# Performance work log

Hardware: AMD Instinct MI355X
Metric: run time of the kernel (lower is better)

The kernel has to match this reference:

```python
import jax, jax.numpy as jnp
import numpy as np

B, T, C, H = 2, 2048, 1024, 16
HS = C // H  # head_size = 64
EPS = 1e-5


def _ln(x, g, b):
    m = jnp.mean(x, axis=-1, keepdims=True)
    v = jnp.mean(jnp.square(x - m), axis=-1, keepdims=True)
    return (x - m) * jax.lax.rsqrt(v + EPS) * g + b


def setup_inputs() -> dict:
    key = jax.random.key(0)
    ks = jax.random.split(key, 16)
    s = lambda k, shape, fan: jax.random.normal(k, shape, jnp.float32) * (fan ** -0.5)
    return {
        "x": jax.random.normal(ks[0], (B, T, C), jnp.float32),
        "Wq": s(ks[1], (H, C, HS), C), "bq": jnp.zeros((H, HS), jnp.float32),
        "Wk": s(ks[2], (H, C, HS), C), "bk": jnp.zeros((H, HS), jnp.float32),
        "Wv": s(ks[3], (H, C, HS), C), "bv": jnp.zeros((H, HS), jnp.float32),
        "Wo": s(ks[4], (C, C), C), "bo": jnp.zeros((C,), jnp.float32),
        "g1": jnp.ones((C,), jnp.float32), "b1": jnp.zeros((C,), jnp.float32),
        "g2": jnp.ones((C,), jnp.float32), "b2": jnp.zeros((C,), jnp.float32),
        "W1": s(ks[5], (C, C), C), "bf1": jnp.zeros((C,), jnp.float32),
        "W2": s(ks[6], (C, C), C), "bf2": jnp.zeros((C,), jnp.float32),
    }


def _block(x, Wq, bq, Wk, bk, Wv, bv, Wo, bo, g1, b1, g2, b2, W1, bf1, W2, bf2):
    h = _ln(x, g1, b1)
    # per-head projections, batched over heads: (B,T,C) x (H,C,HS) -> (B,H,T,HS)
    q = jnp.einsum('btc,hcd->bhtd', h, Wq) + bq[None, :, None, :]
    k = jnp.einsum('btc,hcd->bhtd', h, Wk) + bk[None, :, None, :]
    v = jnp.einsum('btc,hcd->bhtd', h, Wv) + bv[None, :, None, :]
    w = jnp.einsum('bhqd,bhkd->bhqk', q, k) * (HS ** -0.5)
    causal = jnp.tril(jnp.ones((T, T), bool))  # tril[q,k]==0 -> -inf
    w = jnp.where(causal[None, None], w, -jnp.inf)
    # FAITHFUL quirk: original uses F.softmax(w, dim=1) on (B,T,T),
    # i.e. normalization over the QUERY axis (axis=2 of bhqk).
    w = jax.nn.softmax(w, axis=2)
    att = jnp.einsum('bhqk,bhkd->bhqd', w, v)
    att = att.transpose(0, 2, 1, 3).reshape(x.shape[0], x.shape[1], -1)  # concat heads
    x = x + att @ Wo + bo
    h2 = _ln(x, g2, b2)
    x = x + jax.nn.relu(h2 @ W1 + bf1) @ W2 + bf2
    return x


def reference(x, Wq, bq, Wk, bk, Wv, bv, Wo, bo, g1, b1, g2, b2, W1, bf1, W2, bf2):
    return _block(x, Wq, bq, Wk, bk, Wv, bv, Wo, bo, g1, b1, g2, b2, W1, bf1, W2, bf2)
```

## Files before the change

kernel.cpp:

```cpp
#include <hip/hip_runtime.h>
#include <hip/hip_bf16.h>
#include <math.h>


#define B_   2
#define T_   2048
#define C_   1024
#define H_   16
#define HS_  64
#define NROWS 4096
#define C3   3072
#define K1C  0.1803368801111244f

typedef unsigned short ushort_t;
typedef __attribute__((ext_vector_type(8))) short short8;
typedef __attribute__((ext_vector_type(4))) float f32x4;
typedef __attribute__((ext_vector_type(16))) float f32x16;

__device__ __forceinline__ ushort_t f2bf(float f) {
  __hip_bfloat16 h = __float2bfloat16(f);
  ushort_t u; __builtin_memcpy(&u, &h, 2); return u;
}
__device__ __forceinline__ float bf2f(ushort_t u) {
  union { unsigned u; float f; } v; v.u = ((unsigned)u) << 16;
  return v.f;
}
__device__ __forceinline__ unsigned pk2(float a, float b) {
  __hip_bfloat162 t = __float22bfloat162_rn(make_float2(a, b));
  unsigned u; __builtin_memcpy(&u, &t, 4); return u;
}
__device__ __forceinline__ unsigned pkhw(float a, float b) {
  unsigned u;
  asm("v_cvt_pk_bf16_f32 %0, %1, %2" : "=v"(u) : "v"(a), "v"(b));
  return u;
}
__device__ __forceinline__ short8 mk8(unsigned a, unsigned b, unsigned c, unsigned d) {
  union { unsigned u[4]; short8 s; } t;
  t.u[0] = a; t.u[1] = b; t.u[2] = c; t.u[3] = d; return t.s;
}
__device__ __forceinline__ void pl32swap(unsigned &a, unsigned &b) {
  asm("v_permlane32_swap_b32 %0, %1" : "+v"(a), "+v"(b));
}
__device__ __forceinline__ f32x4 mfma16(short8 a, short8 b, f32x4 c) {
  return __builtin_amdgcn_mfma_f32_16x16x32_bf16(a, b, c, 0, 0, 0);
}
__device__ __forceinline__ f32x16 mfma32(short8 a, short8 b, f32x16 c) {
  return __builtin_amdgcn_mfma_f32_32x32x16_bf16(a, b, c, 0, 0, 0);
}
typedef const __attribute__((address_space(1))) void g_void;
typedef __attribute__((address_space(3))) void l_void;
__device__ __forceinline__ void gl_lds16(const void* g, void* l) {
  __builtin_amdgcn_global_load_lds((g_void*)g, (l_void*)l, 16, 0, 0);
}

__global__ __launch_bounds__(256) void ln_bf16(
    const float* __restrict__ x, const float* __restrict__ g,
    const float* __restrict__ b, ushort_t* __restrict__ out) {
  int row = blockIdx.x;
  const float* xr = x + (size_t)row * C_;
  int t = threadIdx.x;
  float4 v = ((const float4*)xr)[t];
  float s  = v.x + v.y + v.z + v.w;
  float ss = v.x*v.x + v.y*v.y + v.z*v.z + v.w*v.w;
  #pragma unroll
  for (int off = 32; off > 0; off >>= 1) {
    s  += __shfl_down(s, off);
    ss += __shfl_down(ss, off);
  }
  __shared__ float red[2][4];
  int wid = t >> 6, lane = t & 63;
  if (lane == 0) { red[0][wid] = s; red[1][wid] = ss; }
  __syncthreads();
  if (t == 0) {
    float a = 0, c = 0;
    for (int i = 0; i < 4; i++) { a += red[0][i]; c += red[1][i]; }
    red[0][0] = a; red[1][0] = c;
  }
  __syncthreads();
  float mean = red[0][0] * (1.0f / C_);
  float var  = red[1][0] * (1.0f / C_) - mean * mean;
  float r = rsqrtf(var + 1e-5f);
  float4 gv = ((const float4*)g)[t];
  float4 bv = ((const float4*)b)[t];
  ushort4 o;
  o.x = f2bf((v.x - mean) * r * gv.x + bv.x);
  o.y = f2bf((v.y - mean) * r * gv.y + bv.y);
  o.z = f2bf((v.z - mean) * r * gv.z + bv.z);
  o.w = f2bf((v.w - mean) * r * gv.w + bv.w);
  ((ushort4*)(out + (size_t)row * C_))[t] = o;
}

__global__ __launch_bounds__(256) void prep_weights(
    const float* __restrict__ Wq, const float* __restrict__ Wk,
    const float* __restrict__ Wv, const float* __restrict__ Wo,
    const float* __restrict__ W1, const float* __restrict__ W2,
    const float* __restrict__ bq, const float* __restrict__ bk,
    const float* __restrict__ bv, ushort_t* __restrict__ Wqkvt,
    ushort_t* __restrict__ Wot3, float* __restrict__ bqkv) {
  int bid = blockIdx.x;
  if (bid < 12288) {
    int idx = bid * 256 + threadIdx.x;
    int n = idx >> 10, c = idx & 1023;
    int sel = n >> 10, nn = n & 1023;
    const float* W = (sel == 0) ? Wq : ((sel == 1) ? Wk : Wv);
    Wqkvt[idx] = f2bf(W[((size_t)(nn >> 6) * C_ + c) * HS_ + (nn & 63)]);
  } else if (bid < 24576) {
    int idx = (bid - 12288) * 256 + threadIdx.x;
    int sel = idx >> 20, rem = idx & 1048575;
    int n = rem >> 10, k = rem & 1023;
    const float* W = (sel == 0) ? Wo : ((sel == 1) ? W1 : W2);
    Wot3[idx] = f2bf(W[(size_t)k * C_ + n]);
  } else {
    int i = (bid - 24576) * 256 + threadIdx.x;
    if (i < 3072)
      bqkv[i] = (i < 1024) ? bq[i] : ((i < 2048) ? bk[i - 1024] : bv[i - 2048]);
  }
}

__global__ __launch_bounds__(256) void gemm128q(
    const ushort_t* __restrict__ A, const ushort_t* __restrict__ Bt,
    const float* __restrict__ bias, ushort_t* __restrict__ Cm,
    int M, int N, int K) {
  __shared__ ushort_t As[128 * 32];
  __shared__ ushort_t Bs[128 * 32];
  int t = threadIdx.x;
  int m0 = blockIdx.y * 128, n0 = blockIdx.x * 128;
  int w = t >> 6, l = t & 63;
  int wr = w >> 1, wc = w & 1;
  int lo = l & 15, hi = l >> 4;
  f32x4 acc[4][4] = {};
  int srow = t >> 2, scol = (t & 3) * 8;
  const ushort_t* Ag = A  + (size_t)(m0 + srow) * K + scol;
  const ushort_t* Bg = Bt + (size_t)(n0 + srow) * K + scol;
  ushort_t* AsP = As + t * 8;
  ushort_t* BsP = Bs + t * 8;
  for (int k0 = 0; k0 < K; k0 += 32) {
    gl_lds16(Ag + k0,          AsP);
    gl_lds16(Ag + 64 * K + k0, AsP + 64 * 32);
    gl_lds16(Bg + k0,          BsP);
    gl_lds16(Bg + 64 * K + k0, BsP + 64 * 32);
    __syncthreads();
    short8 af[4], bfr[4];
    #pragma unroll
    for (int i = 0; i < 4; i++)
      af[i] = *(const short8*)&As[(wr * 64 + i * 16 + lo) * 32 + hi * 8];
    #pragma unroll
    for (int j = 0; j < 4; j++)
      bfr[j] = *(const short8*)&Bs[(wc * 64 + j * 16 + lo) * 32 + hi * 8];
    #pragma unroll
    for (int i = 0; i < 4; i++)
      #pragma unroll
      for (int j = 0; j < 4; j++)
        acc[i][j] = mfma16(af[i], bfr[j], acc[i][j]);
    __syncthreads();
  }
  float qs = (n0 < C_) ? K1C : 1.0f;
  #pragma unroll
  for (int i = 0; i < 4; i++) {
    int m = m0 + wr * 64 + i * 16 + hi * 4;
    #pragma unroll
    for (int j = 0; j < 4; j++) {
      int n = n0 + wc * 64 + j * 16 + lo;
      float bv = bias[n];
      #pragma unroll
      for (int r = 0; r < 4; r++)
        Cm[(size_t)(m + r) * N + n] = f2bf((acc[i][j][r] + bv) * qs);
    }
  }
}

template<int OUT_BF16, int RELU, int HAS_RES>
__global__ __launch_bounds__(256) void gemm64(
    const ushort_t* __restrict__ A, const ushort_t* __restrict__ Bt,
    const float* __restrict__ bias, const float* __restrict__ res,
    void* __restrict__ Cm, int M, int N, int K) {
  __shared__ ushort_t As[128 * 32];
  __shared__ ushort_t Bs[64 * 32];
  int t = threadIdx.x;
  int m0 = blockIdx.y * 128, n0 = blockIdx.x * 64;
  int w = t >> 6, l = t & 63;
  int wr = w >> 1, wc = w & 1;
  int lo = l & 15, hi = l >> 4;
  f32x4 acc[4][2] = {};
  int srow = t >> 2, scol = (t & 3) * 8;
  const ushort_t* Ag = A  + (size_t)(m0 + srow) * K + scol;
  const ushort_t* Bg = Bt + (size_t)(n0 + srow) * K + scol;
  ushort_t* AsP = As + t * 8;
  ushort_t* BsP = Bs + t * 8;
  for (int k0 = 0; k0 < K; k0 += 32) {
    gl_lds16(Ag + k0,          AsP);
    gl_lds16(Ag + 64 * K + k0, AsP + 64 * 32);
    gl_lds16(Bg + k0,          BsP);
    __syncthreads();
    short8 af[4], bfr[2];
    #pragma unroll
    for (int i = 0; i < 4; i++)
      af[i] = *(const short8*)&As[(wr * 64 + i * 16 + lo) * 32 + hi * 8];
    #pragma unroll
    for (int j = 0; j < 2; j++)
      bfr[j] = *(const short8*)&Bs[(wc * 32 + j * 16 + lo) * 32 + hi * 8];
    #pragma unroll
    for (int i = 0; i < 4; i++)
      #pragma unroll
      for (int j = 0; j < 2; j++)
        acc[i][j] = mfma16(af[i], bfr[j], acc[i][j]);
    __syncthreads();
  }
  #pragma unroll
  for (int i = 0; i < 4; i++) {
    int m = m0 + wr * 64 + i * 16 + hi * 4;
    #pragma unroll
    for (int j = 0; j < 2; j++) {
      int n = n0 + wc * 32 + j * 16 + lo;
      float bv = bias[n];
      #pragma unroll
      for (int r = 0; r < 4; r++) {
        float v = acc[i][j][r] + bv;
        if (HAS_RES) v += res[(size_t)(m + r) * N + n];
        if (RELU) v = fmaxf(v, 0.f);
        if (OUT_BF16) ((ushort_t*)Cm)[(size_t)(m + r) * N + n] = f2bf(v);
        else          ((float*)Cm)[(size_t)(m + r) * N + n] = v;
      }
    }
  }
}

__global__ __launch_bounds__(256) void attn_stats(
    const ushort_t* __restrict__ QKV, float* __restrict__ dinv) {
  int bid = blockIdx.x;
  int xcd = bid & 7, loc = (bid >> 3) & 31, half = bid >> 8;
  int bh = xcd * 4 + (loc & 3);
  int j = loc >> 2;
  int kb = half ? (15 - j) : j;
  int b = bh >> 4, h = bh & 15;
  int t = threadIdx.x, w = t >> 6, l = t & 63, l31 = l & 31, hi32 = l >> 5;
  __shared__ ushort_t Qs[2][32 * 64];
  const ushort_t* Qb = QKV + (size_t)b * T_ * C3 + h * HS_;
  const ushort_t* Kb = Qb + C_;
  int k0w = kb * 128 + w * 32;
  short8 ka[4];
  #pragma unroll
  for (int c = 0; c < 4; c++)
    ka[c] = *(const short8*)(Kb + (size_t)(k0w + l31) * C3 + c * 16 + hi32 * 8);
  float s[16];
  #pragma unroll
  for (int r = 0; r < 16; r++) s[r] = 0.f;

  int qoff[4];
  #pragma unroll
  for (int c = 0; c < 4; c++)
    qoff[c] = l31 * 64 + ((c * 2 + hi32) ^ (l31 & 7)) * 8;
  const ushort_t* Q0 = &Qs[0][0];

  int sr = t >> 3, slot = t & 7, su = slot ^ (sr & 7);
  const ushort_t* Qsrc = Qb + (size_t)sr * C3 + su * 8;
  int qt0 = kb * 4, cnt = 64 - qt0;
  int dqt = qt0 + w;

  gl_lds16(Qsrc + (size_t)qt0 * 32 * C3, &Qs[0][t * 8]);
  for (int i = 0; i < cnt; i++) {
    int qt = qt0 + i, cur = i & 1;
    if (i + 1 < cnt) {
      gl_lds16(Qsrc + (size_t)(qt + 1) * 32 * C3, &Qs[cur ^ 1][t * 8]);
      asm volatile("s_waitcnt vmcnt(1)");
    } else {
      asm volatile("s_waitcnt vmcnt(0)");
    }
    __builtin_amdgcn_s_barrier();
    __builtin_amdgcn_sched_barrier(0);
    if (qt >= dqt) {
      int cb = cur << 11;
      short8 qf[4];
      #pragma unroll
      for (int c = 0; c < 4; c++)
        qf[c] = *(const short8*)(Q0 + cb + qoff[c]);
      __builtin_amdgcn_s_setprio(1);
      f32x16 d = {};
      #pragma unroll
      for (int c = 0; c < 4; c++) d = mfma32(ka[c], qf[c], d);
      __builtin_amdgcn_s_setprio(0);
      if (qt == dqt) {
        int qq = qt * 32 + l31;
        #pragma unroll
        for (int r = 0; r < 16; r++) {
          int k = k0w + (r & 3) + 8 * (r >> 2) + 4 * hi32;
          s[r] += (qq >= k) ? __builtin_amdgcn_exp2f(d[r]) : 0.f;
        }
      } else {
        #pragma unroll
        for (int r = 0; r < 16; r++) s[r] += __builtin_amdgcn_exp2f(d[r]);
      }
    }
    __builtin_amdgcn_sched_barrier(0);
    __builtin_amdgcn_s_barrier();
    __builtin_amdgcn_sched_barrier(0);
  }
  #pragma unroll
  for (int off = 1; off < 32; off <<= 1)
    #pragma unroll
    for (int r = 0; r < 16; r++)
      s[r] += __shfl_xor(s[r], off);
  if (l31 == 0) {
    #pragma unroll
    for (int r = 0; r < 16; r++) {
      int k = k0w + (r & 3) + 8 * (r >> 2) + 4 * hi32;
      dinv[(size_t)bh * T_ + k] = 1.0f / s[r];
    }
  }
}

__global__ __launch_bounds__(256) void transpose_v(
    const ushort_t* __restrict__ QKV, const float* __restrict__ dinv,
    ushort_t* __restrict__ Vt) {
  int t0 = blockIdx.x * 64;
  int bh = blockIdx.y; int b = bh >> 4, h = bh & 15;
  __shared__ ushort_t tile[64][65];
  int tid = threadIdx.x;
  #pragma unroll
  for (int i = 0; i < 16; i++) {
    int idx = i * 256 + tid;
    int tt = idx >> 6, dd = idx & 63;
    float v = bf2f(QKV[(size_t)(b * T_ + t0 + tt) * C3 + 2 * C_ + h * HS_ + dd]);
    tile[tt][dd] = f2bf(v * dinv[(size_t)bh * T_ + t0 + tt]);
  }
  __syncthreads();
  #pragma unroll
  for (int i = 0; i < 16; i++) {
    int idx = i * 256 + tid;
    int dd = idx >> 6, tt = idx & 63;
    Vt[((size_t)(bh * HS_ + dd)) * T_ + t0 + tt] = tile[tt][dd];
  }
}

__global__ __launch_bounds__(256) void attn_pv(
    const ushort_t* __restrict__ QKV, const ushort_t* __restrict__ Vt,
    ushort_t* __restrict__ att) {
  int bid = blockIdx.x;
  int xcd = bid & 7, loc = (bid >> 3) & 31, half = bid >> 8;
  int bh = xcd * 4 + (loc & 3);
  int j = loc >> 2;
  int qb = half ? j : (15 - j);
  int b = bh >> 4, h = bh & 15;
  int t = threadIdx.x, w = t >> 6, l = t & 63, l31 = l & 31, hi32 = l >> 5;
  __shared__ ushort_t KV[2][2][32 * 64];
  const ushort_t* Qb = QKV + (size_t)b * T_ * C3 + h * HS_;
  const ushort_t* Kb = Qb + C_;
  const ushort_t* Vb = Vt + (size_t)bh * HS_ * T_;
  int q0w = qb * 128 + w * 32;
  short8 qf[4];
  #pragma unroll
  for (int c = 0; c < 4; c++)
    qf[c] = *(const short8*)(Qb + (size_t)(q0w + l31) * C3 + c * 16 + hi32 * 8);
  f32x16 o0 = {}, o1 = {};
  int nkt = qb * 4 + 4;
  int dkt = q0w >> 5;

  int koff[4], voff[4];
  #pragma unroll
  for (int c = 0; c < 4; c++)
    koff[c] = l31 * 64 + ((c * 2 + hi32) ^ (l31 & 7)) * 8;
  #pragma unroll
  for (int i = 0; i < 4; i++) {
    int u = (i & 1) * 4 + (i >> 1) * 2 + hi32;
    voff[i] = 2048 + l31 * 64 + (u ^ (l31 & 7)) * 8;
  }
  const ushort_t* KV0 = &KV[0][0][0];

  int sr = t >> 3, slot = t & 7, su = slot ^ (sr & 7);
  int vdh = su >> 2, vc2 = su & 3;
  const ushort_t* Ksrc = Kb + (size_t)sr * C3 + su * 8;
  const ushort_t* Vsrc = Vb + (size_t)(vdh * 32 + sr) * T_ + vc2 * 8;

  gl_lds16(Ksrc, &KV[0][0][t * 8]);
  gl_lds16(Vsrc, &KV[0][1][t * 8]);
  for (int kt = 0; kt < nkt; kt++) {
    int cur = kt & 1;
    if (kt + 1 < nkt) {
      gl_lds16(Ksrc + (size_t)(kt + 1) * 32 * C3, &KV[cur ^ 1][0][t * 8]);
      gl_lds16(Vsrc + (kt + 1) * 32,              &KV[cur ^ 1][1][t * 8]);
      asm volatile("s_waitcnt vmcnt(2)");
    } else {
      asm volatile("s_waitcnt vmcnt(0)");
    }
    __builtin_amdgcn_s_barrier();
    __builtin_amdgcn_sched_barrier(0);
    if (kt <= dkt) {
      int cb = cur << 12;
      short8 ka[4], vf[4];
      #pragma unroll
      for (int c = 0; c < 4; c++)
        ka[c] = *(const short8*)(KV0 + cb + koff[c]);
      #pragma unroll
      for (int i = 0; i < 4; i++)
        vf[i] = *(const short8*)(KV0 + cb + voff[i]);
      __builtin_amdgcn_s_setprio(1);
      f32x16 sacc = {};
      #pragma unroll
      for (int c = 0; c < 4; c++) sacc = mfma32(ka[c], qf[c], sacc);
      __builtin_amdgcn_s_setprio(0);
      float e[16];
      if (kt == dkt) {
        int qq = q0w + l31;
        #pragma unroll
        for (int r = 0; r < 16; r++) {
          int k = kt * 32 + (r & 3) + 8 * (r >> 2) + 4 * hi32;
          e[r] = (k <= qq) ? __builtin_amdgcn_exp2f(sacc[r]) : 0.f;
        }
      } else {
        #pragma unroll
        for (int r = 0; r < 16; r++) e[r] = __builtin_amdgcn_exp2f(sacc[r]);
      }
      unsigned u[8];
      #pragma unroll
      for (int j2 = 0; j2 < 8; j2++) u[j2] = pkhw(e[2 * j2], e[2 * j2 + 1]);
      pl32swap(u[0], u[2]); pl32swap(u[1], u[3]);
      pl32swap(u[4], u[6]); pl32swap(u[5], u[7]);
      short8 pa0 = mk8(u[0], u[1], u[2], u[3]);
      short8 pa1 = mk8(u[4], u[5], u[6], u[7]);
      __builtin_amdgcn_s_setprio(1);
      o0 = mfma32(pa0, vf[0], o0);
      o1 = mfma32(pa0, vf[1], o1);
      o0 = mfma32(pa1, vf[2], o0);
      o1 = mfma32(pa1, vf[3], o1);
      __builtin_amdgcn_s_setprio(0);
    }
    __builtin_amdgcn_sched_barrier(0);
    __builtin_amdgcn_s_barrier();
    __builtin_amdgcn_sched_barrier(0);
  }

  #pragma unroll
  for (int r = 0; r < 16; r++) {
    int qq = q0w + (r & 3) + 8 * (r >> 2) + 4 * hi32;
    size_t base = (size_t)(b * T_ + qq) * C_ + h * HS_;
    att[base + l31]      = f2bf(o0[r]);
    att[base + 32 + l31] = f2bf(o1[r]);
  }
}

extern "C" void kernel_launch(void* const* d_in, const int* in_sizes, int n_in,
                              void* d_out, int out_size, void* d_ws, size_t ws_size,
                              hipStream_t stream) {
  const float* x   = (const float*)d_in[0];
  const float* Wq  = (const float*)d_in[1];
  const float* bq  = (const float*)d_in[2];
  const float* Wk  = (const float*)d_in[3];
  const float* bk  = (const float*)d_in[4];
  const float* Wv  = (const float*)d_in[5];
  const float* bv  = (const float*)d_in[6];
  const float* Wo  = (const float*)d_in[7];
  const float* bo  = (const float*)d_in[8];
  const float* g1  = (const float*)d_in[9];
  const float* b1  = (const float*)d_in[10];
  const float* g2  = (const float*)d_in[11];
  const float* b2  = (const float*)d_in[12];
  const float* W1  = (const float*)d_in[13];
  const float* bf1 = (const float*)d_in[14];
  const float* W2  = (const float*)d_in[15];
  const float* bf2 = (const float*)d_in[16];
  float* out = (float*)d_out;

  char* base = (char*)d_ws;
  const size_t MB = 1 << 20;
  ushort_t* QKVb  = (ushort_t*)(base);
  ushort_t* hb    = (ushort_t*)(base + 24 * MB);
  ushort_t* Vt    = (ushort_t*)(base + 32 * MB);
  float*    y     = (float*)   (base + 40 * MB);
  ushort_t* Wqkvt = (ushort_t*)(base + 56 * MB);
  ushort_t* Wot   = (ushort_t*)(base + 62 * MB);
  ushort_t* W1t   = (ushort_t*)(base + 64 * MB);
  ushort_t* W2t   = (ushort_t*)(base + 66 * MB);
  float*    bqkv  = (float*)   (base + 68 * MB);
  float*    dinv  = (float*)   (base + 68 * MB + 65536);

  prep_weights<<<24588, 256, 0, stream>>>(Wq, Wk, Wv, Wo, W1, W2,
                                          bq, bk, bv, Wqkvt, Wot, bqkv);

  ln_bf16<<<NROWS, 256, 0, stream>>>(x, g1, b1, hb);

  gemm128q<<<dim3(C3 / 128, NROWS / 128), 256, 0, stream>>>(
      hb, Wqkvt, bqkv, QKVb, NROWS, C3, C_);

  attn_stats<<<512, 256, 0, stream>>>(QKVb, dinv);
  transpose_v<<<dim3(T_ / 64, 32), 256, 0, stream>>>(QKVb, dinv, Vt);
  ushort_t* attb = hb;
  attn_pv<<<512, 256, 0, stream>>>(QKVb, Vt, attb);

  dim3 g64(C_ / 64, NROWS / 128);
  gemm64<0,0,1><<<g64, 256, 0, stream>>>(attb, Wot, bo, x, y, NROWS, C_, C_);

  ushort_t* h2b = QKVb;
  ln_bf16<<<NROWS, 256, 0, stream>>>(y, g2, b2, h2b);
  ushort_t* f1b = Vt;
  gemm64<1,1,0><<<g64, 256, 0, stream>>>(h2b, W1t, bf1, nullptr, f1b, NROWS, C_, C_);
  gemm64<0,0,1><<<g64, 256, 0, stream>>>(f1b, W2t, bf2, y, out, NROWS, C_, C_);
}
```

Before: 219.8 us.

## Process two tiles per barrier in attention kernels and swizzle QKV GEMM blocks per XCD

Both attention kernels now load two 32-row Q or K/V tiles per pipeline stage and process them in an unrolled pair. This halves the number of block-wide barriers and waitcnt stalls per tile, at the cost of doubled LDS usage. The QKV GEMM also moves from a 2D grid to a 1D grid with a mapping that gives each XCD a contiguous 8x12 block region, aiming for better L2 reuse. The unused pk2 helper is removed.

```diff
diff --git a/kernel.cpp b/kernel.cpp
--- a/kernel.cpp
+++ b/kernel.cpp
@@ -24,10 +24,6 @@
 __device__ __forceinline__ float bf2f(ushort_t u) {
   union { unsigned u; float f; } v; v.u = ((unsigned)u) << 16;
   return v.f;
-}
-__device__ __forceinline__ unsigned pk2(float a, float b) {
-  __hip_bfloat162 t = __float22bfloat162_rn(make_float2(a, b));
-  unsigned u; __builtin_memcpy(&u, &t, 4); return u;
 }
 __device__ __forceinline__ unsigned pkhw(float a, float b) {
   unsigned u;
@@ -124,7 +120,11 @@
   __shared__ ushort_t As[128 * 32];
   __shared__ ushort_t Bs[128 * 32];
   int t = threadIdx.x;
-  int m0 = blockIdx.y * 128, n0 = blockIdx.x * 128;
+  int bid = blockIdx.x;
+  int xcd = bid & 7, loc = bid >> 3;
+  int mb = (xcd >> 1) * 8 + (loc & 7);
+  int nb = (xcd & 1) * 12 + (loc >> 3);
+  int m0 = mb * 128, n0 = nb * 128;
   int w = t >> 6, l = t & 63;
   int wr = w >> 1, wc = w & 1;
   int lo = l & 15, hi = l >> 4;
@@ -234,7 +234,7 @@
   int kb = half ? (15 - j) : j;
   int b = bh >> 4, h = bh & 15;
   int t = threadIdx.x, w = t >> 6, l = t & 63, l31 = l & 31, hi32 = l >> 5;
-  __shared__ ushort_t Qs[2][32 * 64];
+  __shared__ ushort_t Qs[2][2][2048];
   const ushort_t* Qb = QKV + (size_t)b * T_ * C3 + h * HS_;
   const ushort_t* Kb = Qb + C_;
   int k0w = kb * 128 + w * 32;
@@ -250,45 +250,50 @@
   #pragma unroll
   for (int c = 0; c < 4; c++)
     qoff[c] = l31 * 64 + ((c * 2 + hi32) ^ (l31 & 7)) * 8;
-  const ushort_t* Q0 = &Qs[0][0];
 
   int sr = t >> 3, slot = t & 7, su = slot ^ (sr & 7);
   const ushort_t* Qsrc = Qb + (size_t)sr * C3 + su * 8;
   int qt0 = kb * 4, cnt = 64 - qt0;
   int dqt = qt0 + w;
 
-  gl_lds16(Qsrc + (size_t)qt0 * 32 * C3, &Qs[0][t * 8]);
-  for (int i = 0; i < cnt; i++) {
-    int qt = qt0 + i, cur = i & 1;
-    if (i + 1 < cnt) {
-      gl_lds16(Qsrc + (size_t)(qt + 1) * 32 * C3, &Qs[cur ^ 1][t * 8]);
-      asm volatile("s_waitcnt vmcnt(1)");
+  gl_lds16(Qsrc + (size_t)qt0 * 32 * C3,       &Qs[0][0][t * 8]);
+  gl_lds16(Qsrc + (size_t)(qt0 + 1) * 32 * C3, &Qs[0][1][t * 8]);
+  for (int i = 0; i < cnt; i += 2) {
+    int buf = (i >> 1) & 1;
+    if (i + 2 < cnt) {
+      gl_lds16(Qsrc + (size_t)(qt0 + i + 2) * 32 * C3, &Qs[buf ^ 1][0][t * 8]);
+      gl_lds16(Qsrc + (size_t)(qt0 + i + 3) * 32 * C3, &Qs[buf ^ 1][1][t * 8]);
+      asm volatile("s_waitcnt vmcnt(2)");
     } else {
       asm volatile("s_waitcnt vmcnt(0)");
     }
     __builtin_amdgcn_s_barrier();
     __builtin_amdgcn_sched_barrier(0);
-    if (qt >= dqt) {
-      int cb = cur << 11;
-      short8 qf[4];
-      #pragma unroll
-      for (int c = 0; c < 4; c++)
-        qf[c] = *(const short8*)(Q0 + cb + qoff[c]);
-      __builtin_amdgcn_s_setprio(1);
-      f32x16 d = {};
-      #pragma unroll
-      for (int c = 0; c < 4; c++) d = mfma32(ka[c], qf[c], d);
-      __builtin_amdgcn_s_setprio(0);
-      if (qt == dqt) {
-        int qq = qt * 32 + l31;
+    #pragma unroll
+    for (int sub = 0; sub < 2; sub++) {
+      int qt = qt0 + i + sub;
+      if (qt >= dqt) {
+        const ushort_t* base = &Qs[buf][sub][0];
+        short8 qf[4];
         #pragma unroll
-        for (int r = 0; r < 16; r++) {
-          int k = k0w + (r & 3) + 8 * (r >> 2) + 4 * hi32;
-          s[r] += (qq >= k) ? __builtin_amdgcn_exp2f(d[r]) : 0.f;
+        for (int c = 0; c < 4; c++)
+          qf[c] = *(const short8*)(base + qoff[c]);
+        __builtin_amdgcn_s_setprio(1);
+        f32x16 d = {};
+        #pragma unroll
+        for (int c = 0; c < 4; c++) d = mfma32(ka[c], qf[c], d);
+        __builtin_amdgcn_s_setprio(0);
+        if (qt == dqt) {
+          int qq = qt * 32 + l31;
+          #pragma unroll
+          for (int r = 0; r < 16; r++) {
+            int k = k0w + (r & 3) + 8 * (r >> 2) + 4 * hi32;
+            s[r] += (qq >= k) ? __builtin_amdgcn_exp2f(d[r]) : 0.f;
+          }
+        } else {
+          #pragma unroll
+          for (int r = 0; r < 16; r++) s[r] += __builtin_amdgcn_exp2f(d[r]);
         }
-      } else {
-        #pragma unroll
-        for (int r = 0; r < 16; r++) s[r] += __builtin_amdgcn_exp2f(d[r]);
       }
     }
     __builtin_amdgcn_sched_barrier(0);
@@ -342,7 +347,7 @@
   int qb = half ? j : (15 - j);
   int b = bh >> 4, h = bh & 15;
   int t = threadIdx.x, w = t >> 6, l = t & 63, l31 = l & 31, hi32 = l >> 5;
-  __shared__ ushort_t KV[2][2][32 * 64];
+  __shared__ ushort_t KV[2][2][2][2048];
   const ushort_t* Qb = QKV + (size_t)b * T_ * C3 + h * HS_;
   const ushort_t* Kb = Qb + C_;
   const ushort_t* Vb = Vt + (size_t)bh * HS_ * T_;
@@ -364,65 +369,72 @@
     int u = (i & 1) * 4 + (i >> 1) * 2 + hi32;
     voff[i] = 2048 + l31 * 64 + (u ^ (l31 & 7)) * 8;
   }
-  const ushort_t* KV0 = &KV[0][0][0];
 
   int sr = t >> 3, slot = t & 7, su = slot ^ (sr & 7);
   int vdh = su >> 2, vc2 = su & 3;
   const ushort_t* Ksrc = Kb + (size_t)sr * C3 + su * 8;
   const ushort_t* Vsrc = Vb + (size_t)(vdh * 32 + sr) * T_ + vc2 * 8;
 
-  gl_lds16(Ksrc, &KV[0][0][t * 8]);
-  gl_lds16(Vsrc, &KV[0][1][t * 8]);
-  for (int kt = 0; kt < nkt; kt++) {
-    int cur = kt & 1;
-    if (kt + 1 < nkt) {
-      gl_lds16(Ksrc + (size_t)(kt + 1) * 32 * C3, &KV[cur ^ 1][0][t * 8]);
-      gl_lds16(Vsrc + (kt + 1) * 32,              &KV[cur ^ 1][1][t * 8]);
-      asm volatile("s_waitcnt vmcnt(2)");
+  gl_lds16(Ksrc,                  &KV[0][0][0][t * 8]);
+  gl_lds16(Vsrc,                  &KV[0][0][1][t * 8]);
+  gl_lds16(Ksrc + (size_t)32 * C3, &KV[0][1][0][t * 8]);
+  gl_lds16(Vsrc + 32,             &KV[0][1][1][t * 8]);
+  for (int kt = 0; kt < nkt; kt += 2) {
+    int buf = (kt >> 1) & 1;
+    if (kt + 2 < nkt) {
+      gl_lds16(Ksrc + (size_t)(kt + 2) * 32 * C3, &KV[buf ^ 1][0][0][t * 8]);
+      gl_lds16(Vsrc + (kt + 2) * 32,              &KV[buf ^ 1][0][1][t * 8]);
+      gl_lds16(Ksrc + (size_t)(kt + 3) * 32 * C3, &KV[buf ^ 1][1][0][t * 8]);
+      gl_lds16(Vsrc + (kt + 3) * 32,              &KV[buf ^ 1][1][1][t * 8]);
+      asm volatile("s_waitcnt vmcnt(4)");
     } else {
       asm volatile("s_waitcnt vmcnt(0)");
     }
     __builtin_amdgcn_s_barrier();
     __builtin_amdgcn_sched_barrier(0);
-    if (kt <= dkt) {
-      int cb = cur << 12;
-      short8 ka[4], vf[4];
-      #pragma unroll
-      for (int c = 0; c < 4; c++)
-        ka[c] = *(const short8*)(KV0 + cb + koff[c]);
-      #pragma unroll
-      for (int i = 0; i < 4; i++)
-        vf[i] = *(const short8*)(KV0 + cb + voff[i]);
-      __builtin_amdgcn_s_setprio(1);
-      f32x16 sacc = {};
-      #pragma unroll
-      for (int c = 0; c < 4; c++) sacc = mfma32(ka[c], qf[c], sacc);
-      __builtin_amdgcn_s_setprio(0);
-      float e[16];
-      if (kt == dkt) {
-        int qq = q0w + l31;
+    #pragma unroll
+    for (int sub = 0; sub < 2; sub++) {
+      int kts = kt + sub;
+      if (kts <= dkt) {
+        const ushort_t* base = &KV[buf][sub][0][0];
+        short8 ka[4], vf[4];
         #pragma unroll
-        for (int r = 0; r < 16; r++) {
-          int k = kt * 32 + (r & 3) + 8 * (r >> 2) + 4 * hi32;
-          e[r] = (k <= qq) ? __builtin_amdgcn_exp2f(sacc[r]) : 0.f;
+        for (int c = 0; c < 4; c++)
+          ka[c] = *(const short8*)(base + koff[c]);
+        #pragma unroll
+        for (int i = 0; i < 4; i++)
+          vf[i] = *(const short8*)(base + voff[i]);
+        __builtin_amdgcn_s_setprio(1);
+        f32x16 sacc = {};
+        #pragma unroll
+        for (int c = 0; c < 4; c++) sacc = mfma32(ka[c], qf[c], sacc);
+        __builtin_amdgcn_s_setprio(0);
+        float e[16];
+        if (kts == dkt) {
+          int qq = q0w + l31;
+          #pragma unroll
+          for (int r = 0; r < 16; r++) {
+            int k = kts * 32 + (r & 3) + 8 * (r >> 2) + 4 * hi32;
+            e[r] = (k <= qq) ? __builtin_amdgcn_exp2f(sacc[r]) : 0.f;
+          }
+        } else {
+          #pragma unroll
+          for (int r = 0; r < 16; r++) e[r] = __builtin_amdgcn_exp2f(sacc[r]);
         }
-      } else {
+        unsigned u[8];
         #pragma unroll
-        for (int r = 0; r < 16; r++) e[r] = __builtin_amdgcn_exp2f(sacc[r]);
+        for (int j2 = 0; j2 < 8; j2++) u[j2] = pkhw(e[2 * j2], e[2 * j2 + 1]);
+        pl32swap(u[0], u[2]); pl32swap(u[1], u[3]);
+        pl32swap(u[4], u[6]); pl32swap(u[5], u[7]);
+        short8 pa0 = mk8(u[0], u[1], u[2], u[3]);
+        short8 pa1 = mk8(u[4], u[5], u[6], u[7]);
+        __builtin_amdgcn_s_setprio(1);
+        o0 = mfma32(pa0, vf[0], o0);
+        o1 = mfma32(pa0, vf[1], o1);
+        o0 = mfma32(pa1, vf[2], o0);
+        o1 = mfma32(pa1, vf[3], o1);
+        __builtin_amdgcn_s_setprio(0);
       }
-      unsigned u[8];
-      #pragma unroll
-      for (int j2 = 0; j2 < 8; j2++) u[j2] = pkhw(e[2 * j2], e[2 * j2 + 1]);
-      pl32swap(u[0], u[2]); pl32swap(u[1], u[3]);
-      pl32swap(u[4], u[6]); pl32swap(u[5], u[7]);
-      short8 pa0 = mk8(u[0], u[1], u[2], u[3]);
-      short8 pa1 = mk8(u[4], u[5], u[6], u[7]);
-      __builtin_amdgcn_s_setprio(1);
-      o0 = mfma32(pa0, vf[0], o0);
-      o1 = mfma32(pa0, vf[1], o1);
-      o0 = mfma32(pa1, vf[2], o0);
-      o1 = mfma32(pa1, vf[3], o1);
-      __builtin_amdgcn_s_setprio(0);
     }
     __builtin_amdgcn_sched_barrier(0);
     __builtin_amdgcn_s_barrier();
@@ -478,8 +490,7 @@
 
   ln_bf16<<<NROWS, 256, 0, stream>>>(x, g1, b1, hb);
 
-  gemm128q<<<dim3(C3 / 128, NROWS / 128), 256, 0, stream>>>(
-      hb, Wqkvt, bqkv, QKVb, NROWS, C3, C_);
+  gemm128q<<<768, 256, 0, stream>>>(hb, Wqkvt, bqkv, QKVb, NROWS, C3, C_);
 
   attn_stats<<<512, 256, 0, stream>>>(QKVb, dinv);
   transpose_v<<<dim3(T_ / 64, 32), 256, 0, stream>>>(QKVb, dinv, Vt);
```

Result: faster. 210.4 us (-4.3%).
